# Performance work log

Hardware: AMD Instinct MI355X
Metric: run time of the kernel (lower is better)

## Reference

```python
import jax, jax.numpy as jnp
import numpy as np

B, G, N, C = 8, 16, 1024, 256


def setup_inputs() -> dict:
    key = jax.random.key(0)
    k1, k2, k3, k4, k5 = jax.random.split(key, 5)
    x = jax.random.normal(k1, (B, G, N, C), dtype=jnp.float32)
    vs = jax.random.normal(k2, (B, G, 1, N, 3), dtype=jnp.float32)
    s = 1.0 / np.sqrt(C)
    W_fc = jax.random.normal(k3, (C, C), dtype=jnp.float32) * s   # nn.Linear weight [out,in]
    b_fc = jax.random.normal(k4, (C,), dtype=jnp.float32) * s
    W_vn = jax.random.normal(k5, (C, C), dtype=jnp.float32) * s   # VNLinear weight [out,in], no bias
    return {"x": x, "vs": vs, "W_fc": W_fc, "b_fc": b_fc, "W_vn": W_vn}


def reference(x, vs, W_fc, b_fc, W_vn):
    # q = fc(x): [B,G,N,C]
    q = jnp.einsum('bgnc,oc->bgno', x, W_fc) + b_fc
    # softmax over the point dim N (torch dim=2)
    atten = jax.nn.softmax(q, axis=2)
    xw = atten * x  # [B,G,N,C]
    # torch: expand to [B,G,C,N,3] * vs then sum over N.
    # Equivalent contraction without materializing the 5D tensor:
    v = jnp.squeeze(vs, axis=2)  # [B,G,N,3]
    out = jnp.einsum('bgnc,bgnd->bgcd', xw, v)  # [B,G,C,3]
    # VNLinear: bias-free linear over channel dim, shared across the 3 vector comps
    return jnp.einsum('bgcd,oc->bgod', out, W_vn)  # [B,G,C,3]
```

## Files before the change

### kernel.cpp

```cpp
#include <hip/hip_runtime.h>
#include <hip/hip_bf16.h>


#define NQ 1024
#define CQ 256
#define RT 64
#define NT 16
#define XS 136
#define WB_OFF 131072

typedef __attribute__((ext_vector_type(8))) short bf16x8;
typedef __attribute__((ext_vector_type(4))) float f32x4;

__device__ __forceinline__ ushort2 pk2(float a, float b) {
    __hip_bfloat162 h = __float22bfloat162_rn(make_float2(a, b));
    ushort2 r;
    __builtin_memcpy(&r, &h, sizeof(r));
    return r;
}
__device__ __forceinline__ float bf2f(ushort h) {
    union { unsigned u; float f; } v; v.u = ((unsigned)h) << 16;
    return v.f;
}

__global__ __launch_bounds__(256)
void wfc_cvt(const float* __restrict__ Wfc, ushort* __restrict__ Wb) {
    const int i = blockIdx.x * 256 + threadIdx.x;
    float4 v = reinterpret_cast<const float4*>(Wfc)[i];
    ushort2 a0 = pk2(v.x, v.y), a1 = pk2(v.z, v.w);
    ushort4 pk = { a0.x, a0.y, a1.x, a1.y };
    reinterpret_cast<ushort4*>(Wb)[i] = pk;
}

__global__ __launch_bounds__(256, 4)
void attn_pool_partial(const float* __restrict__ x, const float* __restrict__ vs,
                       const ushort* __restrict__ Wb, float* __restrict__ ws) {
    __shared__ __align__(16) ushort xs[RT * XS];
    __shared__ __align__(16) float  vsm[RT * 3];

    const int t = threadIdx.x;
    const int id = blockIdx.x;
    const int ch = (id >> 3) & 1;
    const int rest = (id & 7) | ((id >> 4) << 3);
    const int bg = rest >> 4;
    const int nt = rest & 15;
    const int n0 = nt * RT;
    const int c0 = ch * 128;

    const int w = t >> 6, lane = t & 63;
    const int quad = lane >> 4, l16 = lane & 15;
    const int cstrip = w * 32;

    const float* xb = x + (size_t)bg * NQ * CQ;
    const float* vb = vs + (size_t)bg * NQ * 3;

    if (t < 48) {
        reinterpret_cast<float4*>(vsm)[t] =
            reinterpret_cast<const float4*>(vb + (size_t)n0 * 3)[t];
    }

    f32x4 acc[4][2];
    #pragma unroll
    for (int m = 0; m < 4; ++m)
        #pragma unroll
        for (int ci = 0; ci < 2; ++ci) acc[m][ci] = (f32x4){0.f, 0.f, 0.f, 0.f};

    const int bcol0 = c0 + cstrip + l16;

    #pragma unroll
    for (int kc = 0; kc < 2; ++kc) {
        const int chk = (kc == 0) ? (ch ^ 1) : ch;
        const int kc0 = chk * 128;
        #pragma unroll
        for (int p = 0; p < 8; ++p) {
            int idx = p * 256 + t;
            int row = idx >> 5, k4 = idx & 31;
            float4 v4 = *reinterpret_cast<const float4*>(
                xb + (size_t)(n0 + row) * CQ + kc0 + k4 * 4);
            ushort2 a0 = pk2(v4.x, v4.y), a1 = pk2(v4.z, v4.w);
            ushort4 pk = { a0.x, a0.y, a1.x, a1.y };
            *reinterpret_cast<ushort4*>(&xs[row * XS + k4 * 4]) = pk;
        }
        __syncthreads();
        #pragma unroll
        for (int ks = 0; ks < 4; ++ks) {
            const int kk = ks * 32 + quad * 8;
            bf16x8 b0 = *reinterpret_cast<const bf16x8*>(
                Wb + (size_t)bcol0 * CQ + kc0 + kk);
            bf16x8 b1 = *reinterpret_cast<const bf16x8*>(
                Wb + (size_t)(bcol0 + 16) * CQ + kc0 + kk);
            #pragma unroll
            for (int m = 0; m < 4; ++m) {
                bf16x8 a = *reinterpret_cast<const bf16x8*>(
                    &xs[(m * 16 + l16) * XS + kk]);
                acc[m][0] = __builtin_amdgcn_mfma_f32_16x16x32_bf16(a, b0, acc[m][0], 0, 0, 0);
                acc[m][1] = __builtin_amdgcn_mfma_f32_16x16x32_bf16(a, b1, acc[m][1], 0, 0, 0);
            }
        }
        if (kc == 0) __syncthreads();
    }

    float rZ[2] = {0.f, 0.f}, rS0[2] = {0.f, 0.f}, rS1[2] = {0.f, 0.f}, rS2[2] = {0.f, 0.f};
    #pragma unroll
    for (int m = 0; m < 4; ++m) {
        const int rbase = m * 16 + quad * 4;
        float v0[4], v1[4], v2[4];
        #pragma unroll
        for (int r = 0; r < 4; ++r) {
            v0[r] = vsm[(rbase + r) * 3 + 0];
            v1[r] = vsm[(rbase + r) * 3 + 1];
            v2[r] = vsm[(rbase + r) * 3 + 2];
        }
        #pragma unroll
        for (int ci = 0; ci < 2; ++ci) {
            const int xc = cstrip + ci * 16 + l16;
            #pragma unroll
            for (int r = 0; r < 4; ++r) {
                float e = __expf(acc[m][ci][r]);
                float xv = bf2f(xs[(rbase + r) * XS + xc]);
                rZ[ci] += e;
                float p = e * xv;
                rS0[ci] = fmaf(p, v0[r], rS0[ci]);
                rS1[ci] = fmaf(p, v1[r], rS1[ci]);
                rS2[ci] = fmaf(p, v2[r], rS2[ci]);
            }
        }
    }

    #pragma unroll
    for (int ci = 0; ci < 2; ++ci) {
        float z = rZ[ci], s0 = rS0[ci], s1 = rS1[ci], s2 = rS2[ci];
        #pragma unroll
        for (int off = 16; off < 64; off <<= 1) {
            z  += __shfl_xor(z,  off);
            s0 += __shfl_xor(s0, off);
            s1 += __shfl_xor(s1, off);
            s2 += __shfl_xor(s2, off);
        }
        if (quad == 0) {
            const int col = c0 + cstrip + ci * 16 + l16;
            float* p = ws + ((size_t)bg * CQ + col) * 4;
            atomicAdd(&p[0], z);
            atomicAdd(&p[1], s0);
            atomicAdd(&p[2], s1);
            atomicAdd(&p[3], s2);
        }
    }
}

__global__ __launch_bounds__(256, 4)
void vn_linear(const float* __restrict__ ws, const float* __restrict__ Wvn,
               float* __restrict__ out) {
    __shared__ float Tsm[CQ][3];
    const int bg = blockIdx.x, t = threadIdx.x;
    {
        f32x4 z4 = *reinterpret_cast<const f32x4*>(ws + ((size_t)bg * CQ + t) * 4);
        float inv = 1.f / z4[0];
        Tsm[t][0] = z4[1] * inv;
        Tsm[t][1] = z4[2] * inv;
        Tsm[t][2] = z4[3] * inv;
    }
    __syncthreads();
    const float* wr = Wvn + (size_t)t * CQ;
    float a0 = 0.f, a1 = 0.f, a2 = 0.f;
    #pragma unroll
    for (int c = 0; c < CQ; c += 4) {
        float4 w4 = *reinterpret_cast<const float4*>(wr + c);
        a0 += w4.x * Tsm[c + 0][0] + w4.y * Tsm[c + 1][0]
            + w4.z * Tsm[c + 2][0] + w4.w * Tsm[c + 3][0];
        a1 += w4.x * Tsm[c + 0][1] + w4.y * Tsm[c + 1][1]
            + w4.z * Tsm[c + 2][1] + w4.w * Tsm[c + 3][1];
        a2 += w4.x * Tsm[c + 0][2] + w4.y * Tsm[c + 1][2]
            + w4.z * Tsm[c + 2][2] + w4.w * Tsm[c + 3][2];
    }
    float* op = out + ((size_t)bg * CQ + t) * 3;
    op[0] = a0; op[1] = a1; op[2] = a2;
}

extern "C" void kernel_launch(void* const* d_in, const int* in_sizes, int n_in,
                              void* d_out, int out_size, void* d_ws, size_t ws_size,
                              hipStream_t stream) {
    const float* x   = (const float*)d_in[0];
    const float* vs  = (const float*)d_in[1];
    const float* Wfc = (const float*)d_in[2];
    const float* Wvn = (const float*)d_in[4];
    float* out = (float*)d_out;
    float* ws  = (float*)d_ws;

    ushort* Wb = (ushort*)(ws + WB_OFF);

    (void)hipMemsetAsync(ws, 0, (size_t)128 * CQ * 4 * sizeof(float), stream);
    wfc_cvt<<<dim3(64), dim3(256), 0, stream>>>(Wfc, Wb);
    attn_pool_partial<<<dim3(4096), dim3(256), 0, stream>>>(x, vs, Wb, ws);
    vn_linear<<<dim3(128), dim3(256), 0, stream>>>(ws, Wvn, out);
}
```

Measured before the change: 252.2 us.

## Prefetch both x K-halves into registers upfront and double-buffer LDS tiles

All global loads for both 128-wide K chunks of x are issued at kernel start into registers (64 extra VGPRs). The two halves go into separate LDS buffers, so the second half's conversion and store overlap the first half's MFMAs, and one barrier is removed. Custom barriers wait only on lgkmcnt instead of a full __syncthreads. The cost is higher register and LDS pressure, which may lower occupancy under launch_bounds(256,4).

```diff
diff --git a/kernel.cpp b/kernel.cpp
--- a/kernel.cpp
+++ b/kernel.cpp
@@ -5,7 +5,6 @@
 #define NQ 1024
 #define CQ 256
 #define RT 64
-#define NT 16
 #define XS 136
 #define WB_OFF 131072
 
@@ -21,6 +20,14 @@
 __device__ __forceinline__ float bf2f(ushort h) {
     union { unsigned u; float f; } v; v.u = ((unsigned)h) << 16;
     return v.f;
+}
+
+__device__ __forceinline__ void bar_lgkm() {
+    __builtin_amdgcn_sched_barrier(0);
+    asm volatile("s_waitcnt lgkmcnt(0)" ::: "memory");
+    __builtin_amdgcn_sched_barrier(0);
+    __builtin_amdgcn_s_barrier();
+    __builtin_amdgcn_sched_barrier(0);
 }
 
 __global__ __launch_bounds__(256)
@@ -35,7 +42,8 @@
 __global__ __launch_bounds__(256, 4)
 void attn_pool_partial(const float* __restrict__ x, const float* __restrict__ vs,
                        const ushort* __restrict__ Wb, float* __restrict__ ws) {
-    __shared__ __align__(16) ushort xs[RT * XS];
+    __shared__ __align__(16) ushort xs0[RT * XS];
+    __shared__ __align__(16) ushort xs1[RT * XS];
     __shared__ __align__(16) float  vsm[RT * 3];
 
     const int t = threadIdx.x;
@@ -54,10 +62,42 @@
     const float* xb = x + (size_t)bg * NQ * CQ;
     const float* vb = vs + (size_t)bg * NQ * 3;
 
-    if (t < 48) {
-        reinterpret_cast<float4*>(vsm)[t] =
-            reinterpret_cast<const float4*>(vb + (size_t)n0 * 3)[t];
-    }
+    const int srow = (t * 8) >> 5 >> 3;
+    (void)srow;
+
+    const int sidx_row[1] = {0}; (void)sidx_row;
+    const bool vload = (t < 48);
+    float4 vreg;
+    if (vload) vreg = reinterpret_cast<const float4*>(vb + (size_t)n0 * 3)[t];
+
+    const int kcA = (ch ^ 1) * 128, kcB = ch * 128;
+    float4 LA[8], LB[8];
+    #pragma unroll
+    for (int p = 0; p < 8; ++p) {
+        const int idx = p * 256 + t;
+        const int row = idx >> 5, k4 = idx & 31;
+        LA[p] = *reinterpret_cast<const float4*>(
+            xb + (size_t)(n0 + row) * CQ + kcA + k4 * 4);
+    }
+    #pragma unroll
+    for (int p = 0; p < 8; ++p) {
+        const int idx = p * 256 + t;
+        const int row = idx >> 5, k4 = idx & 31;
+        LB[p] = *reinterpret_cast<const float4*>(
+            xb + (size_t)(n0 + row) * CQ + kcB + k4 * 4);
+    }
+
+    #pragma unroll
+    for (int p = 0; p < 8; ++p) {
+        const int idx = p * 256 + t;
+        const int row = idx >> 5, k4 = idx & 31;
+        ushort2 a0 = pk2(LA[p].x, LA[p].y), a1 = pk2(LA[p].z, LA[p].w);
+        ushort4 pk = { a0.x, a0.y, a1.x, a1.y };
+        *reinterpret_cast<ushort4*>(&xs0[row * XS + k4 * 4]) = pk;
+    }
+    if (vload) reinterpret_cast<float4*>(vsm)[t] = vreg;
+
+    bar_lgkm();
 
     f32x4 acc[4][2];
     #pragma unroll
@@ -68,36 +108,40 @@
     const int bcol0 = c0 + cstrip + l16;
 
     #pragma unroll
-    for (int kc = 0; kc < 2; ++kc) {
-        const int chk = (kc == 0) ? (ch ^ 1) : ch;
-        const int kc0 = chk * 128;
-        #pragma unroll
-        for (int p = 0; p < 8; ++p) {
-            int idx = p * 256 + t;
-            int row = idx >> 5, k4 = idx & 31;
-            float4 v4 = *reinterpret_cast<const float4*>(
-                xb + (size_t)(n0 + row) * CQ + kc0 + k4 * 4);
-            ushort2 a0 = pk2(v4.x, v4.y), a1 = pk2(v4.z, v4.w);
-            ushort4 pk = { a0.x, a0.y, a1.x, a1.y };
-            *reinterpret_cast<ushort4*>(&xs[row * XS + k4 * 4]) = pk;
-        }
-        __syncthreads();
-        #pragma unroll
-        for (int ks = 0; ks < 4; ++ks) {
-            const int kk = ks * 32 + quad * 8;
-            bf16x8 b0 = *reinterpret_cast<const bf16x8*>(
-                Wb + (size_t)bcol0 * CQ + kc0 + kk);
-            bf16x8 b1 = *reinterpret_cast<const bf16x8*>(
-                Wb + (size_t)(bcol0 + 16) * CQ + kc0 + kk);
-            #pragma unroll
-            for (int m = 0; m < 4; ++m) {
-                bf16x8 a = *reinterpret_cast<const bf16x8*>(
-                    &xs[(m * 16 + l16) * XS + kk]);
-                acc[m][0] = __builtin_amdgcn_mfma_f32_16x16x32_bf16(a, b0, acc[m][0], 0, 0, 0);
-                acc[m][1] = __builtin_amdgcn_mfma_f32_16x16x32_bf16(a, b1, acc[m][1], 0, 0, 0);
-            }
-        }
-        if (kc == 0) __syncthreads();
+    for (int ks = 0; ks < 4; ++ks) {
+        const int kk = ks * 32 + quad * 8;
+        bf16x8 b0 = *reinterpret_cast<const bf16x8*>(Wb + (size_t)bcol0 * CQ + kcA + kk);
+        bf16x8 b1 = *reinterpret_cast<const bf16x8*>(Wb + (size_t)(bcol0 + 16) * CQ + kcA + kk);
+        #pragma unroll
+        for (int m = 0; m < 4; ++m) {
+            bf16x8 a = *reinterpret_cast<const bf16x8*>(&xs0[(m * 16 + l16) * XS + kk]);
+            acc[m][0] = __builtin_amdgcn_mfma_f32_16x16x32_bf16(a, b0, acc[m][0], 0, 0, 0);
+            acc[m][1] = __builtin_amdgcn_mfma_f32_16x16x32_bf16(a, b1, acc[m][1], 0, 0, 0);
+        }
+    }
+
+    #pragma unroll
+    for (int p = 0; p < 8; ++p) {
+        const int idx = p * 256 + t;
+        const int row = idx >> 5, k4 = idx & 31;
+        ushort2 a0 = pk2(LB[p].x, LB[p].y), a1 = pk2(LB[p].z, LB[p].w);
+        ushort4 pk = { a0.x, a0.y, a1.x, a1.y };
+        *reinterpret_cast<ushort4*>(&xs1[row * XS + k4 * 4]) = pk;
+    }
+
+    bar_lgkm();
+
+    #pragma unroll
+    for (int ks = 0; ks < 4; ++ks) {
+        const int kk = ks * 32 + quad * 8;
+        bf16x8 b0 = *reinterpret_cast<const bf16x8*>(Wb + (size_t)bcol0 * CQ + kcB + kk);
+        bf16x8 b1 = *reinterpret_cast<const bf16x8*>(Wb + (size_t)(bcol0 + 16) * CQ + kcB + kk);
+        #pragma unroll
+        for (int m = 0; m < 4; ++m) {
+            bf16x8 a = *reinterpret_cast<const bf16x8*>(&xs1[(m * 16 + l16) * XS + kk]);
+            acc[m][0] = __builtin_amdgcn_mfma_f32_16x16x32_bf16(a, b0, acc[m][0], 0, 0, 0);
+            acc[m][1] = __builtin_amdgcn_mfma_f32_16x16x32_bf16(a, b1, acc[m][1], 0, 0, 0);
+        }
     }
 
     float rZ[2] = {0.f, 0.f}, rS0[2] = {0.f, 0.f}, rS1[2] = {0.f, 0.f}, rS2[2] = {0.f, 0.f};
@@ -117,7 +161,7 @@
             #pragma unroll
             for (int r = 0; r < 4; ++r) {
                 float e = __expf(acc[m][ci][r]);
-                float xv = bf2f(xs[(rbase + r) * XS + xc]);
+                float xv = bf2f(xs1[(rbase + r) * XS + xc]);
                 rZ[ci] += e;
                 float p = e * xv;
                 rS0[ci] = fmaf(p, v0[r], rS0[ci]);
```

After: 230.3 us. 1.1x faster.

## Load full 64x256 x tile per 512-thread block; relayout W_fc for coalesced fragments

Applied to the files above, without the earlier changes.

Each block now covers all 256 output channels for its 64-row tile, using 8 waves. This removes the two-block channel split, so x is read from global memory and converted to bf16 once instead of twice. All x loads are issued into registers before the LDS stores, with a single barrier in place of two. W_fc is rearranged into a k-chunk-major layout so each lane's 8-element B fragment loads are contiguous across columns, and the MFMA loop runs at raised wave priority. In exchange the block needs about twice the LDS and more registers per thread, which may lower occupancy.

```diff
diff --git a/kernel.cpp b/kernel.cpp
--- a/kernel.cpp
+++ b/kernel.cpp
@@ -5,8 +5,7 @@
 #define NQ 1024
 #define CQ 256
 #define RT 64
-#define NT 16
-#define XS 136
+#define XS2 264
 #define WB_OFF 131072
 
 typedef __attribute__((ext_vector_type(8))) short bf16x8;
@@ -23,41 +22,70 @@
     return v.f;
 }
 
+__device__ __forceinline__ void bar_lgkm() {
+    __builtin_amdgcn_sched_barrier(0);
+    asm volatile("s_waitcnt lgkmcnt(0)" ::: "memory");
+    __builtin_amdgcn_sched_barrier(0);
+    __builtin_amdgcn_s_barrier();
+    __builtin_amdgcn_sched_barrier(0);
+}
+
 __global__ __launch_bounds__(256)
-void wfc_cvt(const float* __restrict__ Wfc, ushort* __restrict__ Wb) {
+void wfc_cvt(const float* __restrict__ Wfc, ushort* __restrict__ WbT) {
     const int i = blockIdx.x * 256 + threadIdx.x;
-    float4 v = reinterpret_cast<const float4*>(Wfc)[i];
+    const int o = i >> 6;
+    const int k4 = (i & 63) * 4;
+    float4 v = *reinterpret_cast<const float4*>(Wfc + (size_t)o * CQ + k4);
     ushort2 a0 = pk2(v.x, v.y), a1 = pk2(v.z, v.w);
     ushort4 pk = { a0.x, a0.y, a1.x, a1.y };
-    reinterpret_cast<ushort4*>(Wb)[i] = pk;
-}
-
-__global__ __launch_bounds__(256, 4)
+    *reinterpret_cast<ushort4*>(WbT + ((size_t)(k4 >> 3) * CQ + o) * 8 + (k4 & 7)) = pk;
+}
+
+__global__ __launch_bounds__(512, 4)
 void attn_pool_partial(const float* __restrict__ x, const float* __restrict__ vs,
-                       const ushort* __restrict__ Wb, float* __restrict__ ws) {
-    __shared__ __align__(16) ushort xs[RT * XS];
+                       const ushort* __restrict__ WbT, float* __restrict__ ws) {
+    __shared__ __align__(16) ushort xs[RT * XS2];
     __shared__ __align__(16) float  vsm[RT * 3];
 
     const int t = threadIdx.x;
     const int id = blockIdx.x;
-    const int ch = (id >> 3) & 1;
-    const int rest = (id & 7) | ((id >> 4) << 3);
-    const int bg = rest >> 4;
-    const int nt = rest & 15;
+    const int bg = id >> 4;
+    const int nt = id & 15;
     const int n0 = nt * RT;
-    const int c0 = ch * 128;
 
     const int w = t >> 6, lane = t & 63;
     const int quad = lane >> 4, l16 = lane & 15;
-    const int cstrip = w * 32;
+    const int bcol0 = w * 32 + l16;
 
     const float* xb = x + (size_t)bg * NQ * CQ;
     const float* vb = vs + (size_t)bg * NQ * 3;
 
-    if (t < 48) {
-        reinterpret_cast<float4*>(vsm)[t] =
-            reinterpret_cast<const float4*>(vb + (size_t)n0 * 3)[t];
-    }
+    const bool vload = (t < 48);
+    float4 vreg;
+    if (vload) vreg = reinterpret_cast<const float4*>(vb + (size_t)n0 * 3)[t];
+    __builtin_amdgcn_sched_barrier(0);
+
+    float4 LA[8];
+    #pragma unroll
+    for (int p = 0; p < 8; ++p) {
+        const int idx = p * 512 + t;
+        const int row = idx >> 6, k4 = idx & 63;
+        LA[p] = *reinterpret_cast<const float4*>(
+            xb + (size_t)(n0 + row) * CQ + k4 * 4);
+    }
+    __builtin_amdgcn_sched_barrier(0);
+
+    #pragma unroll
+    for (int p = 0; p < 8; ++p) {
+        const int idx = p * 512 + t;
+        const int row = idx >> 6, k4 = idx & 63;
+        ushort2 a0 = pk2(LA[p].x, LA[p].y), a1 = pk2(LA[p].z, LA[p].w);
+        ushort4 pk = { a0.x, a0.y, a1.x, a1.y };
+        *reinterpret_cast<ushort4*>(&xs[row * XS2 + k4 * 4]) = pk;
+    }
+    if (vload) reinterpret_cast<float4*>(vsm)[t] = vreg;
+
+    bar_lgkm();
 
     f32x4 acc[4][2];
     #pragma unroll
@@ -65,40 +93,21 @@
         #pragma unroll
         for (int ci = 0; ci < 2; ++ci) acc[m][ci] = (f32x4){0.f, 0.f, 0.f, 0.f};
 
-    const int bcol0 = c0 + cstrip + l16;
-
-    #pragma unroll
-    for (int kc = 0; kc < 2; ++kc) {
-        const int chk = (kc == 0) ? (ch ^ 1) : ch;
-        const int kc0 = chk * 128;
-        #pragma unroll
-        for (int p = 0; p < 8; ++p) {
-            int idx = p * 256 + t;
-            int row = idx >> 5, k4 = idx & 31;
-            float4 v4 = *reinterpret_cast<const float4*>(
-                xb + (size_t)(n0 + row) * CQ + kc0 + k4 * 4);
-            ushort2 a0 = pk2(v4.x, v4.y), a1 = pk2(v4.z, v4.w);
-            ushort4 pk = { a0.x, a0.y, a1.x, a1.y };
-            *reinterpret_cast<ushort4*>(&xs[row * XS + k4 * 4]) = pk;
-        }
-        __syncthreads();
-        #pragma unroll
-        for (int ks = 0; ks < 4; ++ks) {
-            const int kk = ks * 32 + quad * 8;
-            bf16x8 b0 = *reinterpret_cast<const bf16x8*>(
-                Wb + (size_t)bcol0 * CQ + kc0 + kk);
-            bf16x8 b1 = *reinterpret_cast<const bf16x8*>(
-                Wb + (size_t)(bcol0 + 16) * CQ + kc0 + kk);
-            #pragma unroll
-            for (int m = 0; m < 4; ++m) {
-                bf16x8 a = *reinterpret_cast<const bf16x8*>(
-                    &xs[(m * 16 + l16) * XS + kk]);
-                acc[m][0] = __builtin_amdgcn_mfma_f32_16x16x32_bf16(a, b0, acc[m][0], 0, 0, 0);
-                acc[m][1] = __builtin_amdgcn_mfma_f32_16x16x32_bf16(a, b1, acc[m][1], 0, 0, 0);
-            }
-        }
-        if (kc == 0) __syncthreads();
-    }
+    __builtin_amdgcn_s_setprio(1);
+    #pragma unroll
+    for (int ks = 0; ks < 8; ++ks) {
+        const int kk = ks * 32 + quad * 8;
+        const size_t fo = (size_t)(ks * 4 + quad) * (CQ * 8);
+        bf16x8 b0 = *reinterpret_cast<const bf16x8*>(WbT + fo + (size_t)bcol0 * 8);
+        bf16x8 b1 = *reinterpret_cast<const bf16x8*>(WbT + fo + (size_t)(bcol0 + 16) * 8);
+        #pragma unroll
+        for (int m = 0; m < 4; ++m) {
+            bf16x8 a = *reinterpret_cast<const bf16x8*>(&xs[(m * 16 + l16) * XS2 + kk]);
+            acc[m][0] = __builtin_amdgcn_mfma_f32_16x16x32_bf16(a, b0, acc[m][0], 0, 0, 0);
+            acc[m][1] = __builtin_amdgcn_mfma_f32_16x16x32_bf16(a, b1, acc[m][1], 0, 0, 0);
+        }
+    }
+    __builtin_amdgcn_s_setprio(0);
 
     float rZ[2] = {0.f, 0.f}, rS0[2] = {0.f, 0.f}, rS1[2] = {0.f, 0.f}, rS2[2] = {0.f, 0.f};
     #pragma unroll
@@ -113,11 +122,11 @@
         }
         #pragma unroll
         for (int ci = 0; ci < 2; ++ci) {
-            const int xc = cstrip + ci * 16 + l16;
+            const int xc = w * 32 + ci * 16 + l16;
             #pragma unroll
             for (int r = 0; r < 4; ++r) {
                 float e = __expf(acc[m][ci][r]);
-                float xv = bf2f(xs[(rbase + r) * XS + xc]);
+                float xv = bf2f(xs[(rbase + r) * XS2 + xc]);
                 rZ[ci] += e;
                 float p = e * xv;
                 rS0[ci] = fmaf(p, v0[r], rS0[ci]);
@@ -138,7 +147,7 @@
             s2 += __shfl_xor(s2, off);
         }
         if (quad == 0) {
-            const int col = c0 + cstrip + ci * 16 + l16;
+            const int col = w * 32 + ci * 16 + l16;
             float* p = ws + ((size_t)bg * CQ + col) * 4;
             atomicAdd(&p[0], z);
             atomicAdd(&p[1], s0);
@@ -187,10 +196,10 @@
     float* out = (float*)d_out;
     float* ws  = (float*)d_ws;
 
-    ushort* Wb = (ushort*)(ws + WB_OFF);
+    ushort* WbT = (ushort*)(ws + WB_OFF);
 
     (void)hipMemsetAsync(ws, 0, (size_t)128 * CQ * 4 * sizeof(float), stream);
-    wfc_cvt<<<dim3(64), dim3(256), 0, stream>>>(Wfc, Wb);
-    attn_pool_partial<<<dim3(4096), dim3(256), 0, stream>>>(x, vs, Wb, ws);
+    wfc_cvt<<<dim3(64), dim3(256), 0, stream>>>(Wfc, WbT);
+    attn_pool_partial<<<dim3(2048), dim3(512), 0, stream>>>(x, vs, WbT, ws);
     vn_linear<<<dim3(128), dim3(256), 0, stream>>>(ws, Wvn, out);
 }
```

Result: faster. 233.6 us (-7.4%).
